# Kernel tuning notes

Measured on AMD Instinct MI355X. Metric: run time of the kernel, lower is better.

The kernel has to match this reference:

```python
import jax, jax.numpy as jnp
import numpy as np

B, T, C, H = 8, 2048, 1024, 1024
SCALE = 1.0 / np.sqrt(H).astype(np.float32)


def setup_inputs() -> dict:
    key = jax.random.key(0)
    kx, kq, kk, kv = jax.random.split(key, 4)
    x = jax.random.normal(kx, (B, T, C), dtype=jnp.float32)
    # Linear(C -> H, bias=False): store weights as [C, H] so y = x @ W
    Wq = jax.random.normal(kq, (C, H), dtype=jnp.float32) * (1.0 / np.sqrt(C))
    Wk = jax.random.normal(kk, (C, H), dtype=jnp.float32) * (1.0 / np.sqrt(C))
    Wv = jax.random.normal(kv, (C, H), dtype=jnp.float32) * (1.0 / np.sqrt(C))
    return {"x": x, "Wq": Wq, "Wk": Wk, "Wv": Wv}


def reference(x, Wq, Wk, Wv):
    # Projections
    Q = jnp.einsum('btc,ch->bth', x, Wq)
    K = jnp.einsum('btc,ch->bth', x, Wk)
    V = jnp.einsum('btc,ch->bth', x, Wv)
    t = x.shape[1]
    # Scaled dot-product scores with causal mask
    attn = jnp.einsum('bqh,bkh->bqk', Q, K) * SCALE  # [B,T,T]
    causal = jnp.tril(jnp.ones((t, t), dtype=bool))
    attn = jnp.where(causal, attn, -jnp.inf)
    scores = jax.nn.softmax(attn, axis=-1)
    # dropout p=0.0 (eval/deterministic) -> identity
    out = jnp.einsum('bqk,bkh->bqh', scores, V)
    return out
```

## Files before the change

kernel.cpp:

```cpp
#include <hip/hip_runtime.h>


#define BM 128
#define BN 128
#define BK 32

typedef __attribute__((ext_vector_type(8))) __bf16 bf16x8;
typedef __attribute__((ext_vector_type(4))) float floatx4;

__device__ __forceinline__ unsigned short f2bf(float f) {
  unsigned int u = __float_as_uint(f);
  u += 0x7fffu + ((u >> 16) & 1u);
  return (unsigned short)(u >> 16);
}
__device__ __forceinline__ float bf2f(unsigned short s) {
  return __uint_as_float(((unsigned int)s) << 16);
}

__device__ __forceinline__ void gload_lds16(const unsigned short* g, unsigned short* l) {
  __builtin_amdgcn_global_load_lds(
      (const __attribute__((address_space(1))) void*)g,
      (__attribute__((address_space(3))) void*)l,
      16, 0, 0);
}

__device__ __forceinline__ void gemm_mainloop(
    const unsigned short* __restrict__ A, int lda,
    const unsigned short* __restrict__ Bt, int ldb,
    int m0, int n0, int kTiles,
    unsigned short* As, unsigned short* Bs,
    floatx4 (&acc)[4][4])
{
  const int tid  = threadIdx.x;
  const int wave = tid >> 6;
  const int lane = tid & 63;
  const int wr = wave >> 1;
  const int wc = wave & 1;

  const int c0 = wave * 2;
  const int c1 = c0 + 1;
  const int r0 = c0 * 16 + (lane >> 2);
  const int r1 = c1 * 16 + (lane >> 2);
  const int ck = (lane & 3) * 8;

  const unsigned short* pA0 = A  + (size_t)(m0 + r0) * lda + ck;
  const unsigned short* pA1 = A  + (size_t)(m0 + r1) * lda + ck;
  const unsigned short* pB0 = Bt + (size_t)(n0 + r0) * ldb + ck;
  const unsigned short* pB1 = Bt + (size_t)(n0 + r1) * ldb + ck;

  unsigned short* lA0 = As + c0 * 512;
  unsigned short* lA1 = As + c1 * 512;
  unsigned short* lB0 = Bs + c0 * 512;
  unsigned short* lB1 = Bs + c1 * 512;

  const int fr = lane & 15;
  const int kq = (lane >> 4) * 8;

  for (int kt = 0; kt < kTiles; ++kt) {
    __syncthreads();
    gload_lds16(pA0, lA0);
    gload_lds16(pA1, lA1);
    gload_lds16(pB0, lB0);
    gload_lds16(pB1, lB1);
    pA0 += BK; pA1 += BK; pB0 += BK; pB1 += BK;
    __syncthreads();

    bf16x8 af[4], bg[4];
#pragma unroll
    for (int i = 0; i < 4; ++i)
      af[i] = *(const bf16x8*)(As + ((wr * 64 + i * 16 + fr) * BK + kq));
#pragma unroll
    for (int j = 0; j < 4; ++j)
      bg[j] = *(const bf16x8*)(Bs + ((wc * 64 + j * 16 + fr) * BK + kq));
#pragma unroll
    for (int i = 0; i < 4; ++i)
#pragma unroll
      for (int j = 0; j < 4; ++j)
        acc[i][j] = __builtin_amdgcn_mfma_f32_16x16x32_bf16(af[i], bg[j], acc[i][j], 0, 0, 0);
  }
}

#define ACC_INIT(acc)                         \
  do {                                        \
    floatx4 z_ = {0.f, 0.f, 0.f, 0.f};        \
    _Pragma("unroll")                         \
    for (int i_ = 0; i_ < 4; ++i_)            \
      _Pragma("unroll")                       \
      for (int j_ = 0; j_ < 4; ++j_)          \
        acc[i_][j_] = z_;                     \
  } while (0)


__global__ void cvt_x_kernel(const float* __restrict__ x, unsigned short* __restrict__ xb) {
  int idx = (blockIdx.x * 256 + threadIdx.x) * 4;
  float4 v = *(const float4*)(x + idx);
  ushort4 o;
  o.x = f2bf(v.x); o.y = f2bf(v.y); o.z = f2bf(v.z); o.w = f2bf(v.w);
  *(ushort4*)(xb + idx) = o;
}

__global__ void cvt_w_kernel(const float* __restrict__ W, unsigned short* __restrict__ Wt) {
  __shared__ unsigned short tile[64][65];
  const int k0 = blockIdx.x * 64, n0 = blockIdx.y * 64;
  const int tid = threadIdx.x, tx = tid & 63, ty = tid >> 6;
#pragma unroll
  for (int r = 0; r < 64; r += 4)
    tile[r + ty][tx] = f2bf(W[(size_t)(k0 + r + ty) * 1024 + (n0 + tx)]);
  __syncthreads();
#pragma unroll
  for (int r = 0; r < 64; r += 4)
    Wt[(size_t)(n0 + r + ty) * 1024 + (k0 + tx)] = tile[tx][r + ty];
}

__global__ void zero_l_kernel(float* __restrict__ l) {
  l[blockIdx.x * 256 + threadIdx.x] = 0.f;
}

__global__ __launch_bounds__(256) void gemm_qkv_kernel(
    const unsigned short* __restrict__ xb,
    const unsigned short* __restrict__ Wt,
    unsigned short* __restrict__ Q,
    unsigned short* __restrict__ K,
    unsigned short* __restrict__ V)
{
  __shared__ __align__(16) unsigned short As[BM * BK];
  __shared__ __align__(16) unsigned short Bs[BN * BK];
  floatx4 acc[4][4];
  ACC_INIT(acc);
  const int m0 = blockIdx.x * BM;
  const int n0 = blockIdx.y * BN;
  gemm_mainloop(xb, 1024, Wt, 1024, m0, n0, 1024 / BK, As, Bs, acc);

  unsigned short* const dsts[3] = {Q, K, V};
  unsigned short* D = dsts[n0 >> 10];
  const int ncol0 = n0 & 1023;

  const int tid = threadIdx.x, wave = tid >> 6, lane = tid & 63;
  const int wr = wave >> 1, wc = wave & 1;
  const int rb = m0 + wr * 64 + ((lane >> 4) << 2);
  const int cb = ncol0 + wc * 64 + (lane & 15);
#pragma unroll
  for (int i = 0; i < 4; ++i)
#pragma unroll
    for (int j = 0; j < 4; ++j)
#pragma unroll
      for (int r = 0; r < 4; ++r)
        D[(size_t)(rb + i * 16 + r) * 1024 + (cb + j * 16)] = f2bf(acc[i][j][r]);
}

__global__ void transpose_v_kernel(const unsigned short* __restrict__ V,
                                   unsigned short* __restrict__ Vt) {
  __shared__ unsigned short tile[64][68];
  const int b = blockIdx.z;
  const int t0 = blockIdx.x * 64, h0 = blockIdx.y * 64;
  const int tid = threadIdx.x;
  const int cx = (tid & 15) * 4;
  const int ry = tid >> 4;
  const unsigned short* Vb = V + (size_t)b * 2048 * 1024;
#pragma unroll
  for (int r = 0; r < 64; r += 16) {
    ushort4 v = *(const ushort4*)(Vb + (size_t)(t0 + r + ry) * 1024 + (h0 + cx));
    *(ushort4*)&tile[r + ry][cx] = v;
  }
  __syncthreads();
  unsigned short* Vtb = Vt + (size_t)b * 1024 * 2048;
#pragma unroll
  for (int r = 0; r < 64; r += 16) {
    const int h = r + ry;
    ushort4 o;
    o.x = tile[cx][h]; o.y = tile[cx + 1][h]; o.z = tile[cx + 2][h]; o.w = tile[cx + 3][h];
    *(ushort4*)(Vtb + (size_t)(h0 + h) * 2048 + (t0 + cx)) = o;
  }
}

__global__ __launch_bounds__(256) void gemm_scores_kernel(
    const unsigned short* __restrict__ Q,
    const unsigned short* __restrict__ K,
    unsigned short* __restrict__ S,
    float* __restrict__ lsum)
{
  const int b = blockIdx.x & 7;
  const int t = blockIdx.x >> 3;
  int mi = (int)((sqrtf(8.f * (float)t + 1.f) - 1.f) * 0.5f);
  while ((mi + 1) * (mi + 2) / 2 <= t) ++mi;
  while (mi * (mi + 1) / 2 > t) --mi;
  const int ni = t - mi * (mi + 1) / 2;
  const int m0 = mi * BM;
  const int n0 = ni * BN;

  __shared__ __align__(16) unsigned short As[BM * BK];
  __shared__ __align__(16) unsigned short Bs[BN * BK];
  floatx4 acc[4][4];
  ACC_INIT(acc);
  const unsigned short* Qb = Q + (size_t)b * 2048 * 1024;
  const unsigned short* Kb = K + (size_t)b * 2048 * 1024;
  gemm_mainloop(Qb, 1024, Kb, 1024, m0, n0, 1024 / BK, As, Bs, acc);

  unsigned short* Sb = S + (size_t)b * 2048 * 2048;
  float* lb = lsum + b * 2048;
  const int tid = threadIdx.x, wave = tid >> 6, lane = tid & 63;
  const int wr = wave >> 1, wc = wave & 1;
  const int rb = m0 + wr * 64 + ((lane >> 4) << 2);
  const int cb = n0 + wc * 64 + (lane & 15);

  float rsum[4][4];
#pragma unroll
  for (int i = 0; i < 4; ++i)
#pragma unroll
    for (int r = 0; r < 4; ++r)
      rsum[i][r] = 0.f;

#pragma unroll
  for (int i = 0; i < 4; ++i)
#pragma unroll
    for (int j = 0; j < 4; ++j)
#pragma unroll
      for (int r = 0; r < 4; ++r) {
        const int tq = rb + i * 16 + r;
        const int tk = cb + j * 16;
        float e = 0.f;
        if (tk <= tq) e = __expf(acc[i][j][r] * 0.03125f);
        const unsigned short h = f2bf(e);
        Sb[(size_t)tq * 2048 + tk] = h;
        rsum[i][r] += bf2f(h);
      }

#pragma unroll
  for (int off = 1; off < 16; off <<= 1)
#pragma unroll
    for (int i = 0; i < 4; ++i)
#pragma unroll
      for (int r = 0; r < 4; ++r)
        rsum[i][r] += __shfl_xor(rsum[i][r], off, 64);

  if ((lane & 15) == 0) {
#pragma unroll
    for (int i = 0; i < 4; ++i)
#pragma unroll
      for (int r = 0; r < 4; ++r)
        atomicAdd(&lb[rb + i * 16 + r], rsum[i][r]);
  }
}

__global__ __launch_bounds__(256) void gemm_pv_kernel(
    const unsigned short* __restrict__ S,
    const unsigned short* __restrict__ Vt,
    const float* __restrict__ lsum,
    float* __restrict__ out)
{
  const int b = blockIdx.x & 7;
  const int r2 = blockIdx.x >> 3;
  const int mi = 15 - (r2 >> 3);
  const int ni = r2 & 7;
  const int m0 = mi * BM;
  const int n0 = ni * BN;

  __shared__ __align__(16) unsigned short As[BM * BK];
  __shared__ __align__(16) unsigned short Bs[BN * BK];
  floatx4 acc[4][4];
  ACC_INIT(acc);
  const unsigned short* Pb = S  + (size_t)b * 2048 * 2048;
  const unsigned short* Vb = Vt + (size_t)b * 1024 * 2048;
  const int kTiles = m0 / BK + BM / BK;
  gemm_mainloop(Pb, 2048, Vb, 2048, m0, n0, kTiles, As, Bs, acc);

  float* Ob = out + (size_t)b * 2048 * 1024;
  const float* lb = lsum + b * 2048;
  const int tid = threadIdx.x, wave = tid >> 6, lane = tid & 63;
  const int wr = wave >> 1, wc = wave & 1;
  const int rb = m0 + wr * 64 + ((lane >> 4) << 2);
  const int cb = n0 + wc * 64 + (lane & 15);

  float inv[4][4];
#pragma unroll
  for (int i = 0; i < 4; ++i)
#pragma unroll
    for (int r = 0; r < 4; ++r)
      inv[i][r] = 1.0f / lb[rb + i * 16 + r];

#pragma unroll
  for (int i = 0; i < 4; ++i)
#pragma unroll
    for (int j = 0; j < 4; ++j)
#pragma unroll
      for (int r = 0; r < 4; ++r)
        Ob[(size_t)(rb + i * 16 + r) * 1024 + (cb + j * 16)] = acc[i][j][r] * inv[i][r];
}


extern "C" void kernel_launch(void* const* d_in, const int* in_sizes, int n_in,
                              void* d_out, int out_size, void* d_ws, size_t ws_size,
                              hipStream_t stream) {
  const float* x  = (const float*)d_in[0];
  const float* Wq = (const float*)d_in[1];
  const float* Wk = (const float*)d_in[2];
  const float* Wv = (const float*)d_in[3];
  float* out = (float*)d_out;

  char* ws = (char*)d_ws;
  unsigned short* xb  = (unsigned short*)(ws);
  unsigned short* Wt  = (unsigned short*)(ws + 33554432ull);
  unsigned short* Q   = (unsigned short*)(ws + 39845888ull);
  unsigned short* K   = (unsigned short*)(ws + 73400320ull);
  unsigned short* V   = (unsigned short*)(ws + 106954752ull);
  unsigned short* Vt  = (unsigned short*)(ws + 140509184ull);
  unsigned short* S   = (unsigned short*)(ws + 174063616ull);
  float*          l   = (float*)ws;

  cvt_x_kernel<<<16384, 256, 0, stream>>>(x, xb);
  dim3 gw(16, 16);
  cvt_w_kernel<<<gw, 256, 0, stream>>>(Wq, Wt);
  cvt_w_kernel<<<gw, 256, 0, stream>>>(Wk, Wt + 1024 * 1024);
  cvt_w_kernel<<<gw, 256, 0, stream>>>(Wv, Wt + 2 * 1024 * 1024);

  gemm_qkv_kernel<<<dim3(128, 24), 256, 0, stream>>>(xb, Wt, Q, K, V);

  transpose_v_kernel<<<dim3(32, 16, 8), 256, 0, stream>>>(V, Vt);
  zero_l_kernel<<<64, 256, 0, stream>>>(l);
  gemm_scores_kernel<<<8 * 136, 256, 0, stream>>>(Q, K, S, l);
  gemm_pv_kernel<<<1024, 256, 0, stream>>>(S, Vt, l, out);
}
```

Before: 385.2 us.

## Fuse V transpose into QKV GEMM epilogue, reorder block mapping, use nontemporal stores

Result: slower. 445.0 us (+15.5%).

```diff
diff --git a/kernel.cpp b/kernel.cpp
--- a/kernel.cpp
+++ b/kernel.cpp
@@ -121,7 +121,7 @@
     const unsigned short* __restrict__ Wt,
     unsigned short* __restrict__ Q,
     unsigned short* __restrict__ K,
-    unsigned short* __restrict__ V)
+    unsigned short* __restrict__ Vt)
 {
   __shared__ __align__(16) unsigned short As[BM * BK];
   __shared__ __align__(16) unsigned short Bs[BN * BK];
@@ -131,45 +131,33 @@
   const int n0 = blockIdx.y * BN;
   gemm_mainloop(xb, 1024, Wt, 1024, m0, n0, 1024 / BK, As, Bs, acc);
 
-  unsigned short* const dsts[3] = {Q, K, V};
-  unsigned short* D = dsts[n0 >> 10];
-  const int ncol0 = n0 & 1023;
-
   const int tid = threadIdx.x, wave = tid >> 6, lane = tid & 63;
   const int wr = wave >> 1, wc = wave & 1;
   const int rb = m0 + wr * 64 + ((lane >> 4) << 2);
-  const int cb = ncol0 + wc * 64 + (lane & 15);
-#pragma unroll
-  for (int i = 0; i < 4; ++i)
-#pragma unroll
-    for (int j = 0; j < 4; ++j)
-#pragma unroll
-      for (int r = 0; r < 4; ++r)
-        D[(size_t)(rb + i * 16 + r) * 1024 + (cb + j * 16)] = f2bf(acc[i][j][r]);
-}
-
-__global__ void transpose_v_kernel(const unsigned short* __restrict__ V,
-                                   unsigned short* __restrict__ Vt) {
-  __shared__ unsigned short tile[64][68];
-  const int b = blockIdx.z;
-  const int t0 = blockIdx.x * 64, h0 = blockIdx.y * 64;
-  const int tid = threadIdx.x;
-  const int cx = (tid & 15) * 4;
-  const int ry = tid >> 4;
-  const unsigned short* Vb = V + (size_t)b * 2048 * 1024;
-#pragma unroll
-  for (int r = 0; r < 64; r += 16) {
-    ushort4 v = *(const ushort4*)(Vb + (size_t)(t0 + r + ry) * 1024 + (h0 + cx));
-    *(ushort4*)&tile[r + ry][cx] = v;
-  }
-  __syncthreads();
-  unsigned short* Vtb = Vt + (size_t)b * 1024 * 2048;
-#pragma unroll
-  for (int r = 0; r < 64; r += 16) {
-    const int h = r + ry;
-    ushort4 o;
-    o.x = tile[cx][h]; o.y = tile[cx + 1][h]; o.z = tile[cx + 2][h]; o.w = tile[cx + 3][h];
-    *(ushort4*)(Vtb + (size_t)(h0 + h) * 2048 + (t0 + cx)) = o;
+  if (n0 < 2048) {
+    unsigned short* D = (n0 < 1024) ? Q : K;
+    const int cb = (n0 & 1023) + wc * 64 + (lane & 15);
+#pragma unroll
+    for (int i = 0; i < 4; ++i)
+#pragma unroll
+      for (int j = 0; j < 4; ++j)
+#pragma unroll
+        for (int r = 0; r < 4; ++r)
+          D[(size_t)(rb + i * 16 + r) * 1024 + (cb + j * 16)] = f2bf(acc[i][j][r]);
+  } else {
+    const int bb = m0 >> 11;
+    const int tl = rb & 2047;
+    unsigned short* Vtb = Vt + (size_t)bb * 1024 * 2048;
+    const int hb = (n0 - 2048) + wc * 64 + (lane & 15);
+#pragma unroll
+    for (int i = 0; i < 4; ++i)
+#pragma unroll
+      for (int j = 0; j < 4; ++j) {
+        ushort4 o;
+        o.x = f2bf(acc[i][j][0]); o.y = f2bf(acc[i][j][1]);
+        o.z = f2bf(acc[i][j][2]); o.w = f2bf(acc[i][j][3]);
+        *(ushort4*)(Vtb + (size_t)(hb + j * 16) * 2048 + (tl + i * 16)) = o;
+      }
   }
 }
 
@@ -179,8 +167,8 @@
     unsigned short* __restrict__ S,
     float* __restrict__ lsum)
 {
-  const int b = blockIdx.x & 7;
-  const int t = blockIdx.x >> 3;
+  const int b = blockIdx.x / 136;
+  const int t = blockIdx.x % 136;
   int mi = (int)((sqrtf(8.f * (float)t + 1.f) - 1.f) * 0.5f);
   while ((mi + 1) * (mi + 2) / 2 <= t) ++mi;
   while (mi * (mi + 1) / 2 > t) --mi;
@@ -221,7 +209,7 @@
         float e = 0.f;
         if (tk <= tq) e = __expf(acc[i][j][r] * 0.03125f);
         const unsigned short h = f2bf(e);
-        Sb[(size_t)tq * 2048 + tk] = h;
+        __builtin_nontemporal_store(h, &Sb[(size_t)tq * 2048 + tk]);
         rsum[i][r] += bf2f(h);
       }
 
@@ -248,10 +236,10 @@
     const float* __restrict__ lsum,
     float* __restrict__ out)
 {
-  const int b = blockIdx.x & 7;
-  const int r2 = blockIdx.x >> 3;
-  const int mi = 15 - (r2 >> 3);
-  const int ni = r2 & 7;
+  const int mi = 15 - (int)(blockIdx.x >> 6);
+  const int rest = blockIdx.x & 63;
+  const int b = rest >> 3;
+  const int ni = rest & 7;
   const int m0 = mi * BM;
   const int n0 = ni * BN;
 
@@ -284,7 +272,8 @@
     for (int j = 0; j < 4; ++j)
 #pragma unroll
       for (int r = 0; r < 4; ++r)
-        Ob[(size_t)(rb + i * 16 + r) * 1024 + (cb + j * 16)] = acc[i][j][r] * inv[i][r];
+        __builtin_nontemporal_store(acc[i][j][r] * inv[i][r],
+            &Ob[(size_t)(rb + i * 16 + r) * 1024 + (cb + j * 16)]);
 }
 
 
@@ -302,7 +291,6 @@
   unsigned short* Wt  = (unsigned short*)(ws + 33554432ull);
   unsigned short* Q   = (unsigned short*)(ws + 39845888ull);
   unsigned short* K   = (unsigned short*)(ws + 73400320ull);
-  unsigned short* V   = (unsigned short*)(ws + 106954752ull);
   unsigned short* Vt  = (unsigned short*)(ws + 140509184ull);
   unsigned short* S   = (unsigned short*)(ws + 174063616ull);
   float*          l   = (float*)ws;
@@ -313,9 +301,8 @@
   cvt_w_kernel<<<gw, 256, 0, stream>>>(Wk, Wt + 1024 * 1024);
   cvt_w_kernel<<<gw, 256, 0, stream>>>(Wv, Wt + 2 * 1024 * 1024);
 
-  gemm_qkv_kernel<<<dim3(128, 24), 256, 0, stream>>>(xb, Wt, Q, K, V);
-
-  transpose_v_kernel<<<dim3(32, 16, 8), 256, 0, stream>>>(V, Vt);
+  gemm_qkv_kernel<<<dim3(128, 24), 256, 0, stream>>>(xb, Wt, Q, K, Vt);
+
   zero_l_kernel<<<64, 256, 0, stream>>>(l);
   gemm_scores_kernel<<<8 * 136, 256, 0, stream>>>(Q, K, S, l);
   gemm_pv_kernel<<<1024, 256, 0, stream>>>(S, Vt, l, out);
```
